# Kernel optimization log

Measured on AMD Instinct MI355X. Metric: run time of the kernel, lower is better.

Reference implementation:

```python
import jax, jax.numpy as jnp
import numpy as np

ALPHA = 1.0  # Student-t degrees of freedom (DEC default)


def setup_inputs() -> dict:
    key = jax.random.key(0)
    k1, k2 = jax.random.split(key)
    N, K, D = 32768, 1000, 1024
    h = jax.random.normal(k1, (N, D), dtype=jnp.float32)
    centroids = jax.random.normal(k2, (K, D), dtype=jnp.float32)
    return {"h": h, "centroids": centroids}


def reference(h, centroids):
    # squared pairwise L2 distance via the GEMM expansion:
    # ||h_i - mu_j||^2 = ||h_i||^2 + ||mu_j||^2 - 2 h_i . mu_j
    h_sq = jnp.sum(h * h, axis=1, keepdims=True)            # [N, 1]
    c_sq = jnp.sum(centroids * centroids, axis=1)           # [K]
    cross = jnp.einsum('nd,kd->nk', h, centroids)           # [N, K]
    d2 = jnp.maximum(h_sq + c_sq[None, :] - 2.0 * cross, 0.0)
    # Student-t kernel soft assignment (DEC):
    # q_ij = (1 + d2/alpha)^(-(alpha+1)/2) / sum_j'
    power = -(ALPHA + 1.0) / 2.0
    q = (1.0 + d2 / ALPHA) ** power                          # [N, K]
    q = q / jnp.sum(q, axis=1, keepdims=True)
    return q
```

## Files before the change

### kernel.cpp

```cpp
#include <hip/hip_runtime.h>


typedef unsigned short u16;
typedef __attribute__((ext_vector_type(8))) short bf16x8;
typedef __attribute__((ext_vector_type(4))) float f32x4;

#define N_ROWS 32768
#define K_CENT 1000
#define KP     1024
#define DDIM   1024
#define NT     32

__device__ __forceinline__ u16 f2bf(float x) {
  unsigned u = __float_as_uint(x);
  u += 0x7fffu + ((u >> 16) & 1u);
  return (u16)(u >> 16);
}

__device__ __forceinline__ void gload_lds16(const u16* g, u16* s) {
  __builtin_amdgcn_global_load_lds((__attribute__((address_space(1))) void*)g,
                                   (__attribute__((address_space(3))) void*)s,
                                   16, 0, 0);
}


__global__ __launch_bounds__(256) void prep_h(const float* __restrict__ h,
                                              u16* __restrict__ hb,
                                              float* __restrict__ hsq,
                                              float* __restrict__ rowsum) {
  const int row = blockIdx.x;
  const int t = threadIdx.x;
  const float4 v = reinterpret_cast<const float4*>(h + (size_t)row * DDIM)[t];
  ushort4 b;
  b.x = f2bf(v.x); b.y = f2bf(v.y); b.z = f2bf(v.z); b.w = f2bf(v.w);
  reinterpret_cast<ushort4*>(hb + (size_t)row * DDIM)[t] = b;
  float ss = v.x * v.x + v.y * v.y + v.z * v.z + v.w * v.w;
#pragma unroll
  for (int m = 1; m < 64; m <<= 1) ss += __shfl_xor(ss, m);
  __shared__ float sbuf[4];
  if ((t & 63) == 0) sbuf[t >> 6] = ss;
  __syncthreads();
  if (t == 0) {
    hsq[row] = sbuf[0] + sbuf[1] + sbuf[2] + sbuf[3];
    rowsum[row] = 0.0f;
  }
}

__global__ __launch_bounds__(256) void prep_c(const float* __restrict__ c,
                                              u16* __restrict__ cb,
                                              float* __restrict__ csq) {
  const int row = blockIdx.x;
  const int t = threadIdx.x;
  if (row < K_CENT) {
    const float4 v = reinterpret_cast<const float4*>(c + (size_t)row * DDIM)[t];
    ushort4 b;
    b.x = f2bf(v.x); b.y = f2bf(v.y); b.z = f2bf(v.z); b.w = f2bf(v.w);
    reinterpret_cast<ushort4*>(cb + (size_t)row * DDIM)[t] = b;
    float ss = v.x * v.x + v.y * v.y + v.z * v.z + v.w * v.w;
#pragma unroll
    for (int m = 1; m < 64; m <<= 1) ss += __shfl_xor(ss, m);
    __shared__ float sbuf[4];
    if ((t & 63) == 0) sbuf[t >> 6] = ss;
    __syncthreads();
    if (t == 0) csq[row] = sbuf[0] + sbuf[1] + sbuf[2] + sbuf[3];
  } else {
    ushort4 z; z.x = z.y = z.z = z.w = 0;
    reinterpret_cast<ushort4*>(cb + (size_t)row * DDIM)[t] = z;
    if (t == 0) csq[row] = 1e30f;
  }
}


__device__ __forceinline__ void stageA(const u16* __restrict__ gA, u16* sA,
                                       int tid, int t) {
#pragma unroll
  for (int i = 0; i < 2; ++i) {
    const int p = tid + i * 512;
    const int g = p ^ ((p >> 3) & 7);
    gload_lds16(gA + (size_t)(g >> 2) * DDIM + t * 32 + (g & 3) * 8,
                sA + (((tid & ~63) + i * 512) << 3));
  }
}
__device__ __forceinline__ void stageB(const u16* __restrict__ gB, u16* sB,
                                       int tid, int t) {
#pragma unroll
  for (int i = 0; i < 2; ++i) {
    const int p = tid + i * 512;
    const int g = p ^ ((p >> 3) & 7);
    gload_lds16(gB + (size_t)(g >> 2) * DDIM + t * 32 + (g & 3) * 8,
                sB + (((tid & ~63) + i * 512) << 3));
  }
}

__global__ __launch_bounds__(512, 2) void gemm_q(const u16* __restrict__ hb,
                                                 const u16* __restrict__ cb,
                                                 const float* __restrict__ hsq,
                                                 const float* __restrict__ csq,
                                                 float* __restrict__ out,
                                                 float* __restrict__ rowsum) {
  __shared__ u16 As[4][8192];
  __shared__ u16 Bs[4][8192];

  const int bid = blockIdx.x;
  const int swz = ((bid & 7) << 6) | (bid >> 3);
  const int bcol = swz & 3;
  const int brow = swz >> 2;

  const int tid = threadIdx.x;
  const int w = tid >> 6;
  const int l = tid & 63;
  const int wm = w >> 2;
  const int wn = w & 3;

  const u16* gA = hb + (size_t)brow * 256 * DDIM;
  const u16* gB = cb + (size_t)bcol * 256 * DDIM;

  stageA(gA, As[0], tid, 0); stageB(gB, Bs[0], tid, 0);
  stageA(gA, As[1], tid, 1); stageB(gB, Bs[1], tid, 1);
  stageA(gA, As[2], tid, 2); stageB(gB, Bs[2], tid, 2);

  int aOff[8], bOff[4];
#pragma unroll
  for (int m = 0; m < 8; ++m) {
    const int row = wm * 128 + m * 16 + (l & 15);
    const int g = (row << 2) | (l >> 4);
    aOff[m] = (g ^ ((g >> 3) & 7)) << 3;
  }
#pragma unroll
  for (int n = 0; n < 4; ++n) {
    const int row = wn * 64 + n * 16 + (l & 15);
    const int g = (row << 2) | (l >> 4);
    bOff[n] = (g ^ ((g >> 3) & 7)) << 3;
  }

  f32x4 acc[8][4] = {};

#define KTILE_BODY(T, VM)                                                      \
  {                                                                            \
    const int s_ = (T) & 3, ns_ = ((T) + 3) & 3;                               \
    asm volatile("s_waitcnt vmcnt(" #VM ")" ::: "memory");                     \
    __builtin_amdgcn_s_barrier();                                              \
    __builtin_amdgcn_sched_barrier(0);                                         \
    const u16* SA_ = As[s_]; const u16* SB_ = Bs[s_];                          \
    bf16x8 aF[4], bF[4];                                                       \
    _Pragma("unroll") for (int n = 0; n < 4; ++n)                              \
        bF[n] = *(const bf16x8*)(SB_ + bOff[n]);                               \
    _Pragma("unroll") for (int m = 0; m < 4; ++m)                              \
        aF[m] = *(const bf16x8*)(SA_ + aOff[m]);                               \
    if ((T) + 3 < NT) stageA(gA, As[ns_], tid, (T) + 3);                       \
    __builtin_amdgcn_s_setprio(1);                                             \
    _Pragma("unroll") for (int m = 0; m < 4; ++m)                              \
      _Pragma("unroll") for (int n = 0; n < 4; ++n)                            \
        acc[m][n] = __builtin_amdgcn_mfma_f32_16x16x32_bf16(aF[m], bF[n],      \
                                                            acc[m][n], 0, 0, 0); \
    __builtin_amdgcn_s_setprio(0);                                             \
    _Pragma("unroll") for (int m = 0; m < 4; ++m)                              \
        aF[m] = *(const bf16x8*)(SA_ + aOff[m + 4]);                           \
    if ((T) + 3 < NT) stageB(gB, Bs[ns_], tid, (T) + 3);                       \
    __builtin_amdgcn_s_setprio(1);                                             \
    _Pragma("unroll") for (int m = 0; m < 4; ++m)                              \
      _Pragma("unroll") for (int n = 0; n < 4; ++n)                            \
        acc[m + 4][n] = __builtin_amdgcn_mfma_f32_16x16x32_bf16(aF[m], bF[n],  \
                                                        acc[m + 4][n], 0, 0, 0); \
    __builtin_amdgcn_s_setprio(0);                                             \
  }

  for (int t = 0; t < NT - 2; ++t) KTILE_BODY(t, 8)
  KTILE_BODY(NT - 2, 4)
  KTILE_BODY(NT - 1, 0)
#undef KTILE_BODY

  const int gi0 = brow * 256 + wm * 128;
  const int gj0 = bcol * 256 + wn * 64;
  const int lr = (l >> 4) << 2;
  const int lc = l & 15;

#pragma unroll
  for (int m = 0; m < 8; ++m) {
    float hs[4];
#pragma unroll
    for (int r = 0; r < 4; ++r) hs[r] = hsq[gi0 + m * 16 + lr + r];
    float rs[4] = {0.f, 0.f, 0.f, 0.f};
#pragma unroll
    for (int n = 0; n < 4; ++n) {
      const int gj = gj0 + n * 16 + lc;
      const float cs = csq[gj];
#pragma unroll
      for (int r = 0; r < 4; ++r) {
        float d2 = hs[r] + cs - 2.0f * acc[m][n][r];
        d2 = fmaxf(d2, 0.0f);
        const float qv = 1.0f / (1.0f + d2);
        rs[r] += qv;
        if (gj < K_CENT)
          out[(size_t)(gi0 + m * 16 + lr + r) * K_CENT + gj] = qv;
      }
    }
#pragma unroll
    for (int r = 0; r < 4; ++r) {
      float v = rs[r];
      v += __shfl_xor(v, 1);
      v += __shfl_xor(v, 2);
      v += __shfl_xor(v, 4);
      v += __shfl_xor(v, 8);
      if (lc == 0) atomicAdd(&rowsum[gi0 + m * 16 + lr + r], v);
    }
  }
}


__global__ __launch_bounds__(256) void norm_k(float* __restrict__ out,
                                              const float* __restrict__ rowsum) {
  const int row = blockIdx.x;
  const int t = threadIdx.x;
  if (t < 250) {
    const float inv = 1.0f / rowsum[row];
    float4* p = reinterpret_cast<float4*>(out) + (size_t)row * 250 + t;
    float4 v = *p;
    v.x *= inv; v.y *= inv; v.z *= inv; v.w *= inv;
    *p = v;
  }
}


extern "C" void kernel_launch(void* const* d_in, const int* in_sizes, int n_in,
                              void* d_out, int out_size, void* d_ws, size_t ws_size,
                              hipStream_t stream) {
  const float* h   = (const float*)d_in[0];
  const float* cen = (const float*)d_in[1];
  float* out = (float*)d_out;
  char* ws = (char*)d_ws;

  u16*   cb     = (u16*)(ws);
  u16*   hb     = (u16*)(ws + 2097152);
  float* hsq    = (float*)(ws + 2097152 + 67108864);
  float* csq    = (float*)(ws + 2097152 + 67108864 + 131072);
  float* rowsum = (float*)(ws + 2097152 + 67108864 + 131072 + 4096);

  prep_c<<<KP, 256, 0, stream>>>(cen, cb, csq);
  prep_h<<<N_ROWS, 256, 0, stream>>>(h, hb, hsq, rowsum);
  gemm_q<<<(N_ROWS / 256) * (KP / 256), 512, 0, stream>>>(hb, cb, hsq, csq, out, rowsum);
  norm_k<<<N_ROWS, 256, 0, stream>>>(out, rowsum);
}
```

Measured before the change: 175.4 us.

## Double-buffer MFMA fragments in registers and prefetch next tile before barrier

```diff
diff --git a/kernel.cpp b/kernel.cpp
--- a/kernel.cpp
+++ b/kernel.cpp
@@ -135,40 +135,60 @@
 
   f32x4 acc[8][4] = {};
 
-#define KTILE_BODY(T, VM)                                                      \
+  asm volatile("s_waitcnt vmcnt(4)" ::: "memory");
+  __builtin_amdgcn_s_barrier();
+  __builtin_amdgcn_sched_barrier(0);
+
+  bf16x8 fAa[4], fBa[4], fAb[4], fBb[4];
+#pragma unroll
+  for (int m = 0; m < 4; ++m) fAa[m] = *(const bf16x8*)(&As[0][0] + aOff[m]);
+#pragma unroll
+  for (int n = 0; n < 4; ++n) fBa[n] = *(const bf16x8*)(&Bs[0][0] + bOff[n]);
+
+#define ITER(T, FAc, FBc, FAn, FBn, VMSTR, PREF, STAGE, SYNC)                  \
   {                                                                            \
-    const int s_ = (T) & 3, ns_ = ((T) + 3) & 3;                               \
-    asm volatile("s_waitcnt vmcnt(" #VM ")" ::: "memory");                     \
-    __builtin_amdgcn_s_barrier();                                              \
-    __builtin_amdgcn_sched_barrier(0);                                         \
-    const u16* SA_ = As[s_]; const u16* SB_ = Bs[s_];                          \
-    bf16x8 aF[4], bF[4];                                                       \
-    _Pragma("unroll") for (int n = 0; n < 4; ++n)                              \
-        bF[n] = *(const bf16x8*)(SB_ + bOff[n]);                               \
+    const int sc_ = (T) & 3, sn_ = ((T) + 1) & 3;                              \
+    bf16x8 fA2[4];                                                             \
     _Pragma("unroll") for (int m = 0; m < 4; ++m)                              \
-        aF[m] = *(const bf16x8*)(SA_ + aOff[m]);                               \
-    if ((T) + 3 < NT) stageA(gA, As[ns_], tid, (T) + 3);                       \
+        fA2[m] = *(const bf16x8*)(&As[sc_][0] + aOff[m + 4]);                  \
+    if (PREF) {                                                                \
+      _Pragma("unroll") for (int m = 0; m < 4; ++m)                            \
+          FAn[m] = *(const bf16x8*)(&As[sn_][0] + aOff[m]);                    \
+      _Pragma("unroll") for (int n = 0; n < 4; ++n)                            \
+          FBn[n] = *(const bf16x8*)(&Bs[sn_][0] + bOff[n]);                    \
+    }                                                                          \
+    if (STAGE) {                                                               \
+      stageA(gA, As[((T) + 3) & 3], tid, (T) + 3);                             \
+      stageB(gB, Bs[((T) + 3) & 3], tid, (T) + 3);                             \
+    }                                                                          \
     __builtin_amdgcn_s_setprio(1);                                             \
     _Pragma("unroll") for (int m = 0; m < 4; ++m)                              \
       _Pragma("unroll") for (int n = 0; n < 4; ++n)                            \
-        acc[m][n] = __builtin_amdgcn_mfma_f32_16x16x32_bf16(aF[m], bF[n],      \
+        acc[m][n] = __builtin_amdgcn_mfma_f32_16x16x32_bf16(FAc[m], FBc[n],    \
                                                             acc[m][n], 0, 0, 0); \
-    __builtin_amdgcn_s_setprio(0);                                             \
-    _Pragma("unroll") for (int m = 0; m < 4; ++m)                              \
-        aF[m] = *(const bf16x8*)(SA_ + aOff[m + 4]);                           \
-    if ((T) + 3 < NT) stageB(gB, Bs[ns_], tid, (T) + 3);                       \
-    __builtin_amdgcn_s_setprio(1);                                             \
     _Pragma("unroll") for (int m = 0; m < 4; ++m)                              \
       _Pragma("unroll") for (int n = 0; n < 4; ++n)                            \
-        acc[m + 4][n] = __builtin_amdgcn_mfma_f32_16x16x32_bf16(aF[m], bF[n],  \
+        acc[m + 4][n] = __builtin_amdgcn_mfma_f32_16x16x32_bf16(fA2[m], FBc[n], \
                                                         acc[m + 4][n], 0, 0, 0); \
     __builtin_amdgcn_s_setprio(0);                                             \
-  }
-
-  for (int t = 0; t < NT - 2; ++t) KTILE_BODY(t, 8)
-  KTILE_BODY(NT - 2, 4)
-  KTILE_BODY(NT - 1, 0)
-#undef KTILE_BODY
+    if (SYNC) {                                                                \
+      __builtin_amdgcn_sched_barrier(0);                                       \
+      asm volatile("s_waitcnt vmcnt(" VMSTR ")" ::: "memory");                 \
+      __builtin_amdgcn_s_barrier();                                            \
+      __builtin_amdgcn_sched_barrier(0);                                       \
+    }                                                                          \
+  }
+
+#pragma unroll 1
+  for (int t = 0; t < NT - 4; t += 2) {
+    ITER(t,     fAa, fBa, fAb, fBb, "4", true, true, true)
+    ITER(t + 1, fAb, fBb, fAa, fBa, "4", true, true, true)
+  }
+  ITER(NT - 4, fAa, fBa, fAb, fBb, "4", true, true,  true)
+  ITER(NT - 3, fAb, fBb, fAa, fBa, "0", true, false, true)
+  ITER(NT - 2, fAa, fBa, fAb, fBb, "0", true, false, false)
+  ITER(NT - 1, fAb, fBb, fAa, fBa, "0", false, false, false)
+#undef ITER
 
   const int gi0 = brow * 256 + wm * 128;
   const int gj0 = bcol * 256 + wn * 64;
```

After: 177.5 us. Within noise of the previous version (+1.2%).
